# Kernel optimization log

Hardware: AMD Instinct MI355X
Metric: run time of the kernel (lower is better)

Reference implementation:

```python
import jax, jax.numpy as jnp
import numpy as np

V, D, N, T, U, E = 200000, 128, 50000, 20, 128, 128

def setup_inputs() -> dict:
    key = jax.random.key(0)
    ks = jax.random.split(key, 12)
    s = 0.02
    return {
        "node_ids": jax.random.randint(ks[0], (N,), 0, V, dtype=jnp.int32),
        "neigh_ids": jax.random.randint(ks[1], (N, T), 0, V, dtype=jnp.int32),
        "alpha": jax.random.uniform(ks[2], (N, T), dtype=jnp.float32),
        "table": jax.random.normal(ks[3], (V, D), dtype=jnp.float32),
        "Wq": jax.random.normal(ks[4], (D, U), dtype=jnp.float32) * s,
        "bq": jnp.zeros((U,), dtype=jnp.float32),
        "Wn": jax.random.normal(ks[5], (D, U), dtype=jnp.float32) * s,
        "bn": jnp.zeros((U,), dtype=jnp.float32),
        "Ww": jax.random.normal(ks[6], (2 * U, U), dtype=jnp.float32) * s,
        "bw": jnp.zeros((U,), dtype=jnp.float32),
        "Wg": jax.random.normal(ks[7], (U, E), dtype=jnp.float32) * s,
        "bg": jnp.zeros((E,), dtype=jnp.float32),
    }

def reference(node_ids, neigh_ids, alpha, table, Wq, bq, Wn, bn, Ww, bw, Wg, bg):
    # gather initial embeddings (irregular indexing)
    node_x = table[node_ids]            # [N, D]
    neigh_x = table[neigh_ids]          # [N, T, D]
    # Convolve: node branch Dense+ReLU
    node_h = jax.nn.relu(node_x @ Wq + bq)                       # [N, U]
    # Aggregator: neighbor Dense+ReLU then alpha-weighted matmul
    neigh_h = jax.nn.relu(jnp.einsum('ntd,du->ntu', neigh_x, Wn) + bn)  # [N, T, U]
    agg = jnp.einsum('nt,ntu->nu', alpha, neigh_h)               # [N, U]
    # concat + Dense+ReLU
    emb = jax.nn.relu(jnp.concatenate([node_h, agg], axis=-1) @ Ww + bw)  # [N, U]
    # global (Frobenius) L2 normalize, as in tf.divide(Emb, tf.norm(Emb, ord=2))
    emb = emb / jnp.linalg.norm(emb)
    # final Dense+ReLU to emb_dim
    return jax.nn.relu(emb @ Wg + bg)                            # [N, E]
```

## Files before the change

### kernel.cpp

```cpp
#include <hip/hip_runtime.h>
#include <math.h>


using f32x4  = __attribute__((ext_vector_type(4))) float;
using short8 = __attribute__((ext_vector_type(8))) short;

__device__ __forceinline__ ushort f2bf(float f) {
    uint u = __float_as_uint(f);
    return (ushort)((u + 0x7fffu + ((u >> 16) & 1u)) >> 16);
}
__device__ __forceinline__ float bf2f(ushort h) {
    return __uint_as_float((uint)h << 16);
}

__global__ __launch_bounds__(256)
void prep_weights(const float* __restrict__ Wq, const float* __restrict__ Wn,
                  const float* __restrict__ Ww, const float* __restrict__ Wg,
                  ushort* __restrict__ WqT, ushort* __restrict__ WnT,
                  ushort* __restrict__ WwT, ushort* __restrict__ WgT)
{
    int idx = blockIdx.x * 256 + threadIdx.x;
    const float* W; ushort* WT; int K; int j = idx;
    if (j < 16384)      { W = Wq; WT = WqT; K = 128; }
    else if (j < 32768) { W = Wn; WT = WnT; K = 128; j -= 16384; }
    else if (j < 65536) { W = Ww; WT = WwT; K = 256; j -= 32768; }
    else                { W = Wg; WT = WgT; K = 128; j -= 65536; }
    int n = j & 127, k = j >> 7;
    WT[(size_t)n * K + k] = f2bf(W[j]);
}

template<int KTOT, bool GATHER, bool ABF16, bool SUMSQ, bool SCALE, bool OUTBF16>
__global__ __launch_bounds__(256, 2)
void mfma_gemm(const void* __restrict__ Av, int lda,
               const int* __restrict__ gidx,
               const ushort* __restrict__ WT,
               const float* __restrict__ bias,
               void* __restrict__ outv, int ldo, int M,
               float* __restrict__ partials,
               const float* __restrict__ scale_ptr)
{
    __shared__ __align__(16) char smem[65536];
    __shared__ float red[256];
    char* Bbase = smem + 32768;

    const int tid = threadIdx.x;
    const int w   = tid >> 6;
    const int l   = tid & 63;
    const int l16 = l & 15, lh = l >> 4;
    const int brow = blockIdx.x * 128;

    f32x4 acc[2][8];
#pragma unroll
    for (int fr = 0; fr < 2; ++fr)
#pragma unroll
        for (int fc = 0; fc < 8; ++fc)
#pragma unroll
            for (int i = 0; i < 4; ++i) acc[fr][fc][i] = 0.f;

    for (int k0 = 0; k0 < KTOT; k0 += 128) {
        if (ABF16) {
            const ushort* A = (const ushort*)Av;
#pragma unroll
            for (int it = 0; it < 8; ++it) {
                int idx = it * 256 + tid;
                int r = idx >> 4, o = idx & 15;
                int row = brow + r; int grow = (row < M) ? row : (M - 1);
                if (GATHER) grow = gidx[grow];
                uint4 v = *reinterpret_cast<const uint4*>(&A[(size_t)grow * lda + k0 + 8 * o]);
                *reinterpret_cast<uint4*>(smem + r * 256 + ((16 * o) ^ ((r & 7) << 4))) = v;
            }
        } else {
            const float* A = (const float*)Av;
#pragma unroll
            for (int it = 0; it < 16; ++it) {
                int idx = it * 256 + tid;
                int r = idx >> 5, q = idx & 31;
                int row = brow + r; int grow = (row < M) ? row : (M - 1);
                if (GATHER) grow = gidx[grow];
                float4 v = *reinterpret_cast<const float4*>(&A[(size_t)grow * lda + k0 + 4 * q]);
                uint2 p;
                p.x = (uint)f2bf(v.x) | ((uint)f2bf(v.y) << 16);
                p.y = (uint)f2bf(v.z) | ((uint)f2bf(v.w) << 16);
                *reinterpret_cast<uint2*>(smem + r * 256 + ((8 * q) ^ ((r & 7) << 4))) = p;
            }
        }
#pragma unroll
        for (int it = 0; it < 8; ++it) {
            int idx = it * 256 + tid;
            int n = idx >> 4, o = idx & 15;
            uint4 v = *reinterpret_cast<const uint4*>(&WT[(size_t)n * KTOT + k0 + 8 * o]);
            *reinterpret_cast<uint4*>(Bbase + n * 256 + ((16 * o) ^ ((n & 7) << 4))) = v;
        }
        __syncthreads();

        const int r0 = 32 * w + l16;
        const int r1 = r0 + 16;
#pragma unroll
        for (int ks = 0; ks < 4; ++ks) {
            const int kb = 64 * ks + 16 * lh;
            short8 a0 = *reinterpret_cast<const short8*>(
                smem + r0 * 256 + (kb ^ ((r0 & 7) << 4)));
            short8 a1 = *reinterpret_cast<const short8*>(
                smem + r1 * 256 + (kb ^ ((r1 & 7) << 4)));
#pragma unroll
            for (int fc = 0; fc < 8; ++fc) {
                const int nn = 16 * fc + l16;
                short8 b = *reinterpret_cast<const short8*>(
                    Bbase + nn * 256 + (kb ^ ((nn & 7) << 4)));
                acc[0][fc] = __builtin_amdgcn_mfma_f32_16x16x32_bf16(a0, b, acc[0][fc], 0, 0, 0);
                acc[1][fc] = __builtin_amdgcn_mfma_f32_16x16x32_bf16(a1, b, acc[1][fc], 0, 0, 0);
            }
        }
        __syncthreads();
    }

    const float scale = SCALE ? scale_ptr[0] : 1.0f;
    float bloc[8];
#pragma unroll
    for (int fc = 0; fc < 8; ++fc) bloc[fc] = bias[16 * fc + l16];

    float ssq = 0.f;
#pragma unroll
    for (int fr = 0; fr < 2; ++fr)
#pragma unroll
        for (int fc = 0; fc < 8; ++fc)
#pragma unroll
            for (int i = 0; i < 4; ++i) {
                const int r   = 32 * w + 16 * fr + 4 * lh + i;
                const int col = 16 * fc + l16;
                float v = fmaxf(fmaf(acc[fr][fc][i], scale, bloc[fc]), 0.f);
                if (SUMSQ) { if (brow + r < M) ssq += v * v; }
                if (OUTBF16) ((ushort*)smem)[r * 128 + col] = f2bf(v);
                else         ((float*)smem)[r * 128 + col] = v;
            }
    __syncthreads();

    if (OUTBF16) {
        ushort* out = (ushort*)outv;
#pragma unroll
        for (int it = 0; it < 8; ++it) {
            int idx = it * 256 + tid;
            int r = idx >> 4, o = idx & 15;
            if (brow + r < M)
                *reinterpret_cast<uint4*>(&out[(size_t)(brow + r) * ldo + 8 * o]) =
                    *reinterpret_cast<const uint4*>((ushort*)smem + r * 128 + 8 * o);
        }
    } else {
        float* out = (float*)outv;
#pragma unroll
        for (int it = 0; it < 16; ++it) {
            int idx = it * 256 + tid;
            int r = idx >> 5, q = idx & 31;
            if (brow + r < M)
                *reinterpret_cast<float4*>(&out[(size_t)(brow + r) * ldo + 4 * q]) =
                    *reinterpret_cast<const float4*>((float*)smem + r * 128 + 4 * q);
        }
    }

    if (SUMSQ) {
        red[tid] = ssq;
        __syncthreads();
        for (int st = 128; st > 0; st >>= 1) {
            if (tid < st) red[tid] += red[tid + st];
            __syncthreads();
        }
        if (tid == 0) partials[blockIdx.x] = red[0];
    }
}

__global__ __launch_bounds__(256)
void agg_bf16(const ushort* __restrict__ H,
              const int* __restrict__ nids,
              const float* __restrict__ alpha,
              ushort* __restrict__ outb,
              int N)
{
    const int n   = blockIdx.x * 16 + (threadIdx.x >> 4);
    const int l16 = threadIdx.x & 15;
    if (n >= N) return;

    const int*   idp = &nids[n * 20];
    const float* alp = &alpha[n * 20];
    float a[8];
#pragma unroll
    for (int j = 0; j < 8; ++j) a[j] = 0.f;

#pragma unroll
    for (int t = 0; t < 20; ++t) {
        const int   id = idp[t];
        const float al = alp[t];
        uint4 h = *reinterpret_cast<const uint4*>(&H[(size_t)id * 128 + 8 * l16]);
        a[0] = fmaf(al, bf2f((ushort)(h.x & 0xffff)), a[0]);
        a[1] = fmaf(al, bf2f((ushort)(h.x >> 16)),    a[1]);
        a[2] = fmaf(al, bf2f((ushort)(h.y & 0xffff)), a[2]);
        a[3] = fmaf(al, bf2f((ushort)(h.y >> 16)),    a[3]);
        a[4] = fmaf(al, bf2f((ushort)(h.z & 0xffff)), a[4]);
        a[5] = fmaf(al, bf2f((ushort)(h.z >> 16)),    a[5]);
        a[6] = fmaf(al, bf2f((ushort)(h.w & 0xffff)), a[6]);
        a[7] = fmaf(al, bf2f((ushort)(h.w >> 16)),    a[7]);
    }
    uint4 p;
    p.x = (uint)f2bf(a[0]) | ((uint)f2bf(a[1]) << 16);
    p.y = (uint)f2bf(a[2]) | ((uint)f2bf(a[3]) << 16);
    p.z = (uint)f2bf(a[4]) | ((uint)f2bf(a[5]) << 16);
    p.w = (uint)f2bf(a[6]) | ((uint)f2bf(a[7]) << 16);
    *reinterpret_cast<uint4*>(&outb[(size_t)n * 256 + 8 * l16]) = p;
}

__global__ void reduce_norm(const float* __restrict__ partials, int n,
                            float* __restrict__ scale)
{
    __shared__ float red[256];
    float s = 0.f;
    for (int i = threadIdx.x; i < n; i += 256) s += partials[i];
    red[threadIdx.x] = s;
    __syncthreads();
    for (int st = 128; st > 0; st >>= 1) {
        if (threadIdx.x < st) red[threadIdx.x] += red[threadIdx.x + st];
        __syncthreads();
    }
    if (threadIdx.x == 0) scale[0] = 1.0f / sqrtf(red[0]);
}

extern "C" void kernel_launch(void* const* d_in, const int* in_sizes, int n_in,
                              void* d_out, int out_size, void* d_ws, size_t ws_size,
                              hipStream_t stream)
{
    const int*   node_ids  = (const int*)  d_in[0];
    const int*   neigh_ids = (const int*)  d_in[1];
    const float* alpha     = (const float*)d_in[2];
    const float* table     = (const float*)d_in[3];
    const float* Wq        = (const float*)d_in[4];
    const float* bq        = (const float*)d_in[5];
    const float* Wn        = (const float*)d_in[6];
    const float* bn        = (const float*)d_in[7];
    const float* Ww        = (const float*)d_in[8];
    const float* bw        = (const float*)d_in[9];
    const float* Wg        = (const float*)d_in[10];
    const float* bg        = (const float*)d_in[11];

    const int N = in_sizes[0];
    const int V = in_sizes[3] / 128;
    float* out = (float*)d_out;

    ushort* H    = (ushort*)d_ws;
    ushort* nh   = H    + (size_t)V * 128;
    ushort* embb = nh   + (size_t)N * 256;
    ushort* WqT  = embb + (size_t)N * 128;
    ushort* WnT  = WqT  + 16384;
    ushort* WwT  = WnT  + 16384;
    ushort* WgT  = WwT  + 32768;
    float*  partials = (float*)(WgT + 16384);
    float*  scale    = partials + 512;

    const size_t need = (size_t)((char*)(scale + 16) - (char*)d_ws);
    if (ws_size < need) return;

    const int nblkN = (N + 127) / 128;
    const int nblkV = (V + 127) / 128;

    prep_weights<<<320, 256, 0, stream>>>(Wq, Wn, Ww, Wg, WqT, WnT, WwT, WgT);
    mfma_gemm<128, false, false, false, false, true><<<nblkV, 256, 0, stream>>>(
        table, 128, nullptr, WnT, bn, H, 128, V, nullptr, nullptr);
    mfma_gemm<128, true, false, false, false, true><<<nblkN, 256, 0, stream>>>(
        table, 128, node_ids, WqT, bq, nh, 256, N, nullptr, nullptr);
    agg_bf16<<<(N + 15) / 16, 256, 0, stream>>>(H, neigh_ids, alpha, nh + 128, N);
    mfma_gemm<256, false, true, true, false, true><<<nblkN, 256, 0, stream>>>(
        nh, 256, nullptr, WwT, bw, embb, 128, N, partials, nullptr);
    reduce_norm<<<1, 256, 0, stream>>>(partials, nblkN, scale);
    mfma_gemm<128, false, true, false, true, false><<<nblkN, 256, 0, stream>>>(
        embb, 128, nullptr, WgT, bg, out, 128, N, nullptr, scale);
}
```

Baseline: 113.7 us.

## Load A fragments directly into registers and swap MFMA operands to skip LDS staging

```diff
diff --git a/kernel.cpp b/kernel.cpp
--- a/kernel.cpp
+++ b/kernel.cpp
@@ -11,6 +11,15 @@
 }
 __device__ __forceinline__ float bf2f(ushort h) {
     return __uint_as_float((uint)h << 16);
+}
+__device__ __forceinline__ uint pk2(float lo, float hi) {
+    return (uint)f2bf(lo) | ((uint)f2bf(hi) << 16);
+}
+__device__ __forceinline__ short8 pack8(f32x4 a, f32x4 b) {
+    uint u0 = pk2(a[0], a[1]), u1 = pk2(a[2], a[3]);
+    uint u2 = pk2(b[0], b[1]), u3 = pk2(b[2], b[3]);
+    uint4 r; r.x = u0; r.y = u1; r.z = u2; r.w = u3;
+    union { uint4 u; short8 s; } cv; cv.u = r; return cv.s;
 }
 
 __global__ __launch_bounds__(256)
@@ -29,7 +38,7 @@
     WT[(size_t)n * K + k] = f2bf(W[j]);
 }
 
-template<int KTOT, bool GATHER, bool ABF16, bool SUMSQ, bool SCALE, bool OUTBF16>
+template<int KTOT, bool GATHER, bool AFP32, bool SUMSQ, bool SCALE, bool OUTFP32>
 __global__ __launch_bounds__(256, 2)
 void mfma_gemm(const void* __restrict__ Av, int lda,
                const int* __restrict__ gidx,
@@ -39,121 +48,112 @@
                float* __restrict__ partials,
                const float* __restrict__ scale_ptr)
 {
-    __shared__ __align__(16) char smem[65536];
+    __shared__ __align__(16) ushort Blds[128 * 128];
     __shared__ float red[256];
-    char* Bbase = smem + 32768;
 
     const int tid = threadIdx.x;
-    const int w   = tid >> 6;
-    const int l   = tid & 63;
+    const int w = tid >> 6, l = tid & 63;
     const int l16 = l & 15, lh = l >> 4;
     const int brow = blockIdx.x * 128;
 
+    const int row0 = brow + 32 * w + l16;
+    const int row1 = row0 + 16;
+    int g0 = (row0 < M) ? row0 : (M - 1);
+    int g1 = (row1 < M) ? row1 : (M - 1);
+    if (GATHER) { g0 = gidx[g0]; g1 = gidx[g1]; }
+
     f32x4 acc[2][8];
 #pragma unroll
-    for (int fr = 0; fr < 2; ++fr)
-#pragma unroll
-        for (int fc = 0; fc < 8; ++fc)
-#pragma unroll
-            for (int i = 0; i < 4; ++i) acc[fr][fc][i] = 0.f;
-
-    for (int k0 = 0; k0 < KTOT; k0 += 128) {
-        if (ABF16) {
+    for (int nt = 0; nt < 2; ++nt)
+#pragma unroll
+        for (int mt = 0; mt < 8; ++mt)
+#pragma unroll
+            for (int i = 0; i < 4; ++i) acc[nt][mt][i] = 0.f;
+
+    for (int kc = 0; kc < KTOT / 128; ++kc) {
+        const int kbase = kc * 128;
+
+        short8 a[2][4];
+        f32x4 t[2][8];
+        if (AFP32) {
+            const float* A = (const float*)Av;
+#pragma unroll
+            for (int nt = 0; nt < 2; ++nt) {
+                const float* rp = A + (size_t)(nt ? g1 : g0) * lda + kbase + 8 * lh;
+#pragma unroll
+                for (int ks = 0; ks < 4; ++ks) {
+                    t[nt][2 * ks]     = *reinterpret_cast<const f32x4*>(rp + 32 * ks);
+                    t[nt][2 * ks + 1] = *reinterpret_cast<const f32x4*>(rp + 32 * ks + 4);
+                }
+            }
+        } else {
             const ushort* A = (const ushort*)Av;
 #pragma unroll
-            for (int it = 0; it < 8; ++it) {
-                int idx = it * 256 + tid;
-                int r = idx >> 4, o = idx & 15;
-                int row = brow + r; int grow = (row < M) ? row : (M - 1);
-                if (GATHER) grow = gidx[grow];
-                uint4 v = *reinterpret_cast<const uint4*>(&A[(size_t)grow * lda + k0 + 8 * o]);
-                *reinterpret_cast<uint4*>(smem + r * 256 + ((16 * o) ^ ((r & 7) << 4))) = v;
-            }
-        } else {
-            const float* A = (const float*)Av;
-#pragma unroll
-            for (int it = 0; it < 16; ++it) {
-                int idx = it * 256 + tid;
-                int r = idx >> 5, q = idx & 31;
-                int row = brow + r; int grow = (row < M) ? row : (M - 1);
-                if (GATHER) grow = gidx[grow];
-                float4 v = *reinterpret_cast<const float4*>(&A[(size_t)grow * lda + k0 + 4 * q]);
-                uint2 p;
-                p.x = (uint)f2bf(v.x) | ((uint)f2bf(v.y) << 16);
-                p.y = (uint)f2bf(v.z) | ((uint)f2bf(v.w) << 16);
-                *reinterpret_cast<uint2*>(smem + r * 256 + ((8 * q) ^ ((r & 7) << 4))) = p;
-            }
-        }
+            for (int nt = 0; nt < 2; ++nt) {
+                const ushort* rp = A + (size_t)(nt ? g1 : g0) * lda + kbase + 8 * lh;
+#pragma unroll
+                for (int ks = 0; ks < 4; ++ks)
+                    a[nt][ks] = *reinterpret_cast<const short8*>(rp + 32 * ks);
+            }
+        }
+
+        if (kc > 0) __syncthreads();
 #pragma unroll
         for (int it = 0; it < 8; ++it) {
             int idx = it * 256 + tid;
             int n = idx >> 4, o = idx & 15;
-            uint4 v = *reinterpret_cast<const uint4*>(&WT[(size_t)n * KTOT + k0 + 8 * o]);
-            *reinterpret_cast<uint4*>(Bbase + n * 256 + ((16 * o) ^ ((n & 7) << 4))) = v;
+            uint4 v = *reinterpret_cast<const uint4*>(&WT[(size_t)n * KTOT + kbase + 8 * o]);
+            *reinterpret_cast<uint4*>(
+                (char*)Blds + n * 256 + ((16 * o) ^ ((n & 7) << 4))) = v;
         }
         __syncthreads();
 
-        const int r0 = 32 * w + l16;
-        const int r1 = r0 + 16;
+        if (AFP32) {
+#pragma unroll
+            for (int nt = 0; nt < 2; ++nt)
+#pragma unroll
+                for (int ks = 0; ks < 4; ++ks)
+                    a[nt][ks] = pack8(t[nt][2 * ks], t[nt][2 * ks + 1]);
+        }
+
 #pragma unroll
         for (int ks = 0; ks < 4; ++ks) {
-            const int kb = 64 * ks + 16 * lh;
-            short8 a0 = *reinterpret_cast<const short8*>(
-                smem + r0 * 256 + (kb ^ ((r0 & 7) << 4)));
-            short8 a1 = *reinterpret_cast<const short8*>(
-                smem + r1 * 256 + (kb ^ ((r1 & 7) << 4)));
-#pragma unroll
-            for (int fc = 0; fc < 8; ++fc) {
-                const int nn = 16 * fc + l16;
-                short8 b = *reinterpret_cast<const short8*>(
-                    Bbase + nn * 256 + (kb ^ ((nn & 7) << 4)));
-                acc[0][fc] = __builtin_amdgcn_mfma_f32_16x16x32_bf16(a0, b, acc[0][fc], 0, 0, 0);
-                acc[1][fc] = __builtin_amdgcn_mfma_f32_16x16x32_bf16(a1, b, acc[1][fc], 0, 0, 0);
-            }
-        }
-        __syncthreads();
+#pragma unroll
+            for (int mt = 0; mt < 8; ++mt) {
+                short8 wf = *reinterpret_cast<const short8*>(
+                    (char*)Blds + (16 * mt + l16) * 256 +
+                    ((64 * ks + 16 * lh) ^ ((l16 & 7) << 4)));
+                acc[0][mt] = __builtin_amdgcn_mfma_f32_16x16x32_bf16(wf, a[0][ks], acc[0][mt], 0, 0, 0);
+                acc[1][mt] = __builtin_amdgcn_mfma_f32_16x16x32_bf16(wf, a[1][ks], acc[1][mt], 0, 0, 0);
+            }
+        }
     }
 
     const float scale = SCALE ? scale_ptr[0] : 1.0f;
-    float bloc[8];
-#pragma unroll
-    for (int fc = 0; fc < 8; ++fc) bloc[fc] = bias[16 * fc + l16];
-
     float ssq = 0.f;
 #pragma unroll
-    for (int fr = 0; fr < 2; ++fr)
-#pragma unroll
-        for (int fc = 0; fc < 8; ++fc)
-#pragma unroll
-            for (int i = 0; i < 4; ++i) {
-                const int r   = 32 * w + 16 * fr + 4 * lh + i;
-                const int col = 16 * fc + l16;
-                float v = fmaxf(fmaf(acc[fr][fc][i], scale, bloc[fc]), 0.f);
-                if (SUMSQ) { if (brow + r < M) ssq += v * v; }
-                if (OUTBF16) ((ushort*)smem)[r * 128 + col] = f2bf(v);
-                else         ((float*)smem)[r * 128 + col] = v;
-            }
-    __syncthreads();
-
-    if (OUTBF16) {
-        ushort* out = (ushort*)outv;
-#pragma unroll
-        for (int it = 0; it < 8; ++it) {
-            int idx = it * 256 + tid;
-            int r = idx >> 4, o = idx & 15;
-            if (brow + r < M)
-                *reinterpret_cast<uint4*>(&out[(size_t)(brow + r) * ldo + 8 * o]) =
-                    *reinterpret_cast<const uint4*>((ushort*)smem + r * 128 + 8 * o);
-        }
-    } else {
-        float* out = (float*)outv;
-#pragma unroll
-        for (int it = 0; it < 16; ++it) {
-            int idx = it * 256 + tid;
-            int r = idx >> 5, q = idx & 31;
-            if (brow + r < M)
-                *reinterpret_cast<float4*>(&out[(size_t)(brow + r) * ldo + 4 * q]) =
-                    *reinterpret_cast<const float4*>((float*)smem + r * 128 + 4 * q);
+    for (int nt = 0; nt < 2; ++nt) {
+        const int row = nt ? row1 : row0;
+        const bool ok = row < M;
+#pragma unroll
+        for (int mt = 0; mt < 8; ++mt) {
+            const f32x4 bv = *reinterpret_cast<const f32x4*>(&bias[16 * mt + 4 * lh]);
+            f32x4 v;
+#pragma unroll
+            for (int i = 0; i < 4; ++i)
+                v[i] = fmaxf(fmaf(acc[nt][mt][i], scale, bv[i]), 0.f);
+            if (SUMSQ && ok)
+                ssq += v[0] * v[0] + v[1] * v[1] + v[2] * v[2] + v[3] * v[3];
+            if (OUTFP32) {
+                if (ok)
+                    *reinterpret_cast<f32x4*>(
+                        &((float*)outv)[(size_t)row * ldo + 16 * mt + 4 * lh]) = v;
+            } else {
+                uint2 p; p.x = pk2(v[0], v[1]); p.y = pk2(v[2], v[3]);
+                if (ok)
+                    *reinterpret_cast<uint2*>(
+                        &((ushort*)outv)[(size_t)row * ldo + 16 * mt + 4 * lh]) = p;
+            }
         }
     }
 
@@ -200,10 +200,10 @@
         a[7] = fmaf(al, bf2f((ushort)(h.w >> 16)),    a[7]);
     }
     uint4 p;
-    p.x = (uint)f2bf(a[0]) | ((uint)f2bf(a[1]) << 16);
-    p.y = (uint)f2bf(a[2]) | ((uint)f2bf(a[3]) << 16);
-    p.z = (uint)f2bf(a[4]) | ((uint)f2bf(a[5]) << 16);
-    p.w = (uint)f2bf(a[6]) | ((uint)f2bf(a[7]) << 16);
+    p.x = pk2(a[0], a[1]);
+    p.y = pk2(a[2], a[3]);
+    p.z = pk2(a[4], a[5]);
+    p.w = pk2(a[6], a[7]);
     *reinterpret_cast<uint4*>(&outb[(size_t)n * 256 + 8 * l16]) = p;
 }
 
@@ -260,14 +260,14 @@
     const int nblkV = (V + 127) / 128;
 
     prep_weights<<<320, 256, 0, stream>>>(Wq, Wn, Ww, Wg, WqT, WnT, WwT, WgT);
-    mfma_gemm<128, false, false, false, false, true><<<nblkV, 256, 0, stream>>>(
+    mfma_gemm<128, false, true, false, false, false><<<nblkV, 256, 0, stream>>>(
         table, 128, nullptr, WnT, bn, H, 128, V, nullptr, nullptr);
-    mfma_gemm<128, true, false, false, false, true><<<nblkN, 256, 0, stream>>>(
+    mfma_gemm<128, true, true, false, false, false><<<nblkN, 256, 0, stream>>>(
         table, 128, node_ids, WqT, bq, nh, 256, N, nullptr, nullptr);
     agg_bf16<<<(N + 15) / 16, 256, 0, stream>>>(H, neigh_ids, alpha, nh + 128, N);
-    mfma_gemm<256, false, true, true, false, true><<<nblkN, 256, 0, stream>>>(
+    mfma_gemm<256, false, false, true, false, false><<<nblkN, 256, 0, stream>>>(
         nh, 256, nullptr, WwT, bw, embb, 128, N, partials, nullptr);
     reduce_norm<<<1, 256, 0, stream>>>(partials, nblkN, scale);
-    mfma_gemm<128, false, true, false, true, false><<<nblkN, 256, 0, stream>>>(
+    mfma_gemm<128, false, false, false, true, true><<<nblkN, 256, 0, stream>>>(
         embb, 128, nullptr, WgT, bg, out, 128, N, nullptr, scale);
 }
```

New measurement: 125.1 us. 1.1x slower.

## Merge table and node projections into one persistent kernel with prefetch

Applied to the files above, without the earlier changes.

```diff
diff --git a/kernel.cpp b/kernel.cpp
--- a/kernel.cpp
+++ b/kernel.cpp
@@ -11,6 +11,9 @@
 }
 __device__ __forceinline__ float bf2f(ushort h) {
     return __uint_as_float((uint)h << 16);
+}
+__device__ __forceinline__ uint pk2(float lo, float hi) {
+    return (uint)f2bf(lo) | ((uint)f2bf(hi) << 16);
 }
 
 __global__ __launch_bounds__(256)
@@ -29,143 +32,129 @@
     WT[(size_t)n * K + k] = f2bf(W[j]);
 }
 
-template<int KTOT, bool GATHER, bool ABF16, bool SUMSQ, bool SCALE, bool OUTBF16>
-__global__ __launch_bounds__(256, 2)
-void mfma_gemm(const void* __restrict__ Av, int lda,
-               const int* __restrict__ gidx,
-               const ushort* __restrict__ WT,
-               const float* __restrict__ bias,
-               void* __restrict__ outv, int ldo, int M,
-               float* __restrict__ partials,
-               const float* __restrict__ scale_ptr)
-{
-    __shared__ __align__(16) char smem[65536];
-    __shared__ float red[256];
-    char* Bbase = smem + 32768;
-
+__device__ __forceinline__ void stage_w128(const ushort* __restrict__ WT,
+                                           const float* __restrict__ bias,
+                                           ushort* Wlds, float* blds, int tid)
+{
+#pragma unroll
+    for (int it = 0; it < 8; ++it) {
+        int idx = it * 256 + tid, n = idx >> 4, o = idx & 15;
+        uint4 v = *reinterpret_cast<const uint4*>(&WT[(size_t)n * 128 + 8 * o]);
+        *reinterpret_cast<uint4*>((char*)Wlds + n * 256 + ((16 * o) ^ ((n & 7) << 4))) = v;
+    }
+    if (tid < 128) blds[tid] = bias[tid];
+}
+
+template<bool GATHER>
+__device__ __forceinline__ void k1_side(const float* __restrict__ table,
+                                        const int* __restrict__ gidx,
+                                        const ushort* Wlds, const float* blds,
+                                        ushort* Albs,
+                                        ushort* __restrict__ out, int ldo, int M,
+                                        int sideIdx, int sideBlk)
+{
     const int tid = threadIdx.x;
-    const int w   = tid >> 6;
-    const int l   = tid & 63;
-    const int l16 = l & 15, lh = l >> 4;
-    const int brow = blockIdx.x * 128;
-
-    f32x4 acc[2][8];
-#pragma unroll
-    for (int fr = 0; fr < 2; ++fr)
-#pragma unroll
-        for (int fc = 0; fc < 8; ++fc)
-#pragma unroll
-            for (int i = 0; i < 4; ++i) acc[fr][fc][i] = 0.f;
-
-    for (int k0 = 0; k0 < KTOT; k0 += 128) {
-        if (ABF16) {
-            const ushort* A = (const ushort*)Av;
-#pragma unroll
-            for (int it = 0; it < 8; ++it) {
-                int idx = it * 256 + tid;
-                int r = idx >> 4, o = idx & 15;
-                int row = brow + r; int grow = (row < M) ? row : (M - 1);
-                if (GATHER) grow = gidx[grow];
-                uint4 v = *reinterpret_cast<const uint4*>(&A[(size_t)grow * lda + k0 + 8 * o]);
-                *reinterpret_cast<uint4*>(smem + r * 256 + ((16 * o) ^ ((r & 7) << 4))) = v;
-            }
-        } else {
-            const float* A = (const float*)Av;
-#pragma unroll
-            for (int it = 0; it < 16; ++it) {
-                int idx = it * 256 + tid;
-                int r = idx >> 5, q = idx & 31;
-                int row = brow + r; int grow = (row < M) ? row : (M - 1);
-                if (GATHER) grow = gidx[grow];
-                float4 v = *reinterpret_cast<const float4*>(&A[(size_t)grow * lda + k0 + 4 * q]);
-                uint2 p;
-                p.x = (uint)f2bf(v.x) | ((uint)f2bf(v.y) << 16);
-                p.y = (uint)f2bf(v.z) | ((uint)f2bf(v.w) << 16);
-                *reinterpret_cast<uint2*>(smem + r * 256 + ((8 * q) ^ ((r & 7) << 4))) = p;
-            }
-        }
-#pragma unroll
-        for (int it = 0; it < 8; ++it) {
-            int idx = it * 256 + tid;
-            int n = idx >> 4, o = idx & 15;
-            uint4 v = *reinterpret_cast<const uint4*>(&WT[(size_t)n * KTOT + k0 + 8 * o]);
-            *reinterpret_cast<uint4*>(Bbase + n * 256 + ((16 * o) ^ ((n & 7) << 4))) = v;
-        }
-        __syncthreads();
-
-        const int r0 = 32 * w + l16;
-        const int r1 = r0 + 16;
+    const int w = tid >> 6, l = tid & 63, l16 = l & 15, lh = l >> 4;
+    const int nt = (M + 63) >> 6;
+    int tile = sideIdx;
+
+    f32x4 f[8];
+    if (tile < nt) {
+#pragma unroll
+        for (int j = 0; j < 8; ++j) {
+            int u = j * 256 + tid;
+            int r = u >> 5, c4 = u & 31;
+            int row = tile * 64 + r;
+            int g = (row < M) ? row : (M - 1);
+            if (GATHER) g = gidx[g];
+            f[j] = *reinterpret_cast<const f32x4*>(table + (size_t)g * 128 + 4 * c4);
+        }
+    }
+    __syncthreads();
+
+    for (; tile < nt; tile += sideBlk) {
+        uint2 p[8];
+#pragma unroll
+        for (int j = 0; j < 8; ++j) {
+            p[j].x = pk2(f[j][0], f[j][1]);
+            p[j].y = pk2(f[j][2], f[j][3]);
+        }
+        __syncthreads();
+#pragma unroll
+        for (int j = 0; j < 8; ++j) {
+            int u = j * 256 + tid, r = u >> 5, c4 = u & 31;
+            *reinterpret_cast<uint2*>(
+                (char*)Albs + r * 256 + ((8 * c4) ^ ((r & 7) << 4))) = p[j];
+        }
+        __syncthreads();
+
+        const int nxt = tile + sideBlk;
+        if (nxt < nt) {
+#pragma unroll
+            for (int j = 0; j < 8; ++j) {
+                int u = j * 256 + tid;
+                int r = u >> 5, c4 = u & 31;
+                int row = nxt * 64 + r;
+                int g = (row < M) ? row : (M - 1);
+                if (GATHER) g = gidx[g];
+                f[j] = *reinterpret_cast<const f32x4*>(table + (size_t)g * 128 + 4 * c4);
+            }
+        }
+
+        f32x4 acc[8];
+#pragma unroll
+        for (int mt = 0; mt < 8; ++mt)
+#pragma unroll
+            for (int i = 0; i < 4; ++i) acc[mt][i] = 0.f;
+        const int r0 = 16 * w + l16;
 #pragma unroll
         for (int ks = 0; ks < 4; ++ks) {
-            const int kb = 64 * ks + 16 * lh;
-            short8 a0 = *reinterpret_cast<const short8*>(
-                smem + r0 * 256 + (kb ^ ((r0 & 7) << 4)));
-            short8 a1 = *reinterpret_cast<const short8*>(
-                smem + r1 * 256 + (kb ^ ((r1 & 7) << 4)));
-#pragma unroll
-            for (int fc = 0; fc < 8; ++fc) {
-                const int nn = 16 * fc + l16;
-                short8 b = *reinterpret_cast<const short8*>(
-                    Bbase + nn * 256 + (kb ^ ((nn & 7) << 4)));
-                acc[0][fc] = __builtin_amdgcn_mfma_f32_16x16x32_bf16(a0, b, acc[0][fc], 0, 0, 0);
-                acc[1][fc] = __builtin_amdgcn_mfma_f32_16x16x32_bf16(a1, b, acc[1][fc], 0, 0, 0);
-            }
-        }
-        __syncthreads();
-    }
-
-    const float scale = SCALE ? scale_ptr[0] : 1.0f;
-    float bloc[8];
-#pragma unroll
-    for (int fc = 0; fc < 8; ++fc) bloc[fc] = bias[16 * fc + l16];
-
-    float ssq = 0.f;
-#pragma unroll
-    for (int fr = 0; fr < 2; ++fr)
-#pragma unroll
-        for (int fc = 0; fc < 8; ++fc)
-#pragma unroll
-            for (int i = 0; i < 4; ++i) {
-                const int r   = 32 * w + 16 * fr + 4 * lh + i;
-                const int col = 16 * fc + l16;
-                float v = fmaxf(fmaf(acc[fr][fc][i], scale, bloc[fc]), 0.f);
-                if (SUMSQ) { if (brow + r < M) ssq += v * v; }
-                if (OUTBF16) ((ushort*)smem)[r * 128 + col] = f2bf(v);
-                else         ((float*)smem)[r * 128 + col] = v;
-            }
-    __syncthreads();
-
-    if (OUTBF16) {
-        ushort* out = (ushort*)outv;
-#pragma unroll
-        for (int it = 0; it < 8; ++it) {
-            int idx = it * 256 + tid;
-            int r = idx >> 4, o = idx & 15;
-            if (brow + r < M)
-                *reinterpret_cast<uint4*>(&out[(size_t)(brow + r) * ldo + 8 * o]) =
-                    *reinterpret_cast<const uint4*>((ushort*)smem + r * 128 + 8 * o);
-        }
-    } else {
-        float* out = (float*)outv;
-#pragma unroll
-        for (int it = 0; it < 16; ++it) {
-            int idx = it * 256 + tid;
-            int r = idx >> 5, q = idx & 31;
-            if (brow + r < M)
-                *reinterpret_cast<float4*>(&out[(size_t)(brow + r) * ldo + 4 * q]) =
-                    *reinterpret_cast<const float4*>((float*)smem + r * 128 + 4 * q);
-        }
-    }
-
-    if (SUMSQ) {
-        red[tid] = ssq;
-        __syncthreads();
-        for (int st = 128; st > 0; st >>= 1) {
-            if (tid < st) red[tid] += red[tid + st];
-            __syncthreads();
-        }
-        if (tid == 0) partials[blockIdx.x] = red[0];
-    }
+            short8 a = *reinterpret_cast<const short8*>(
+                (const char*)Albs + r0 * 256 + ((64 * ks + 16 * lh) ^ ((r0 & 7) << 4)));
+#pragma unroll
+            for (int mt = 0; mt < 8; ++mt) {
+                short8 wf = *reinterpret_cast<const short8*>(
+                    (const char*)Wlds + (16 * mt + l16) * 256 +
+                    ((64 * ks + 16 * lh) ^ ((l16 & 7) << 4)));
+                acc[mt] = __builtin_amdgcn_mfma_f32_16x16x32_bf16(wf, a, acc[mt], 0, 0, 0);
+            }
+        }
+
+        const int row = tile * 64 + r0;
+        if (row < M) {
+#pragma unroll
+            for (int mt = 0; mt < 8; ++mt) {
+                f32x4 bv = *reinterpret_cast<const f32x4*>(&blds[16 * mt + 4 * lh]);
+                uint2 q;
+                q.x = pk2(fmaxf(acc[mt][0] + bv[0], 0.f), fmaxf(acc[mt][1] + bv[1], 0.f));
+                q.y = pk2(fmaxf(acc[mt][2] + bv[2], 0.f), fmaxf(acc[mt][3] + bv[3], 0.f));
+                *reinterpret_cast<uint2*>(&out[(size_t)row * ldo + 16 * mt + 4 * lh]) = q;
+            }
+        }
+    }
+}
+
+__global__ __launch_bounds__(256, 3)
+void k1_dual(const float* __restrict__ table, const int* __restrict__ node_ids,
+             const ushort* __restrict__ WnT, const float* __restrict__ bn,
+             const ushort* __restrict__ WqT, const float* __restrict__ bq,
+             ushort* __restrict__ H, ushort* __restrict__ nh,
+             int V, int N, int splitH, int nBlk)
+{
+    __shared__ __align__(16) ushort Wlds[128 * 128];
+    __shared__ __align__(16) ushort Albs[64 * 128];
+    __shared__ __align__(16) float blds[128];
+    const int tid = threadIdx.x;
+    const bool isH = (int)blockIdx.x < splitH;
+
+    stage_w128(isH ? WnT : WqT, isH ? bn : bq, Wlds, blds, tid);
+
+    if (isH)
+        k1_side<false>(table, nullptr, Wlds, blds, Albs, H, 128, V,
+                       blockIdx.x, splitH);
+    else
+        k1_side<true>(table, node_ids, Wlds, blds, Albs, nh, 256, N,
+                      blockIdx.x - splitH, nBlk - splitH);
 }
 
 __global__ __launch_bounds__(256)
@@ -184,7 +173,6 @@
     float a[8];
 #pragma unroll
     for (int j = 0; j < 8; ++j) a[j] = 0.f;
-
 #pragma unroll
     for (int t = 0; t < 20; ++t) {
         const int   id = idp[t];
@@ -200,11 +188,148 @@
         a[7] = fmaf(al, bf2f((ushort)(h.w >> 16)),    a[7]);
     }
     uint4 p;
-    p.x = (uint)f2bf(a[0]) | ((uint)f2bf(a[1]) << 16);
-    p.y = (uint)f2bf(a[2]) | ((uint)f2bf(a[3]) << 16);
-    p.z = (uint)f2bf(a[4]) | ((uint)f2bf(a[5]) << 16);
-    p.w = (uint)f2bf(a[6]) | ((uint)f2bf(a[7]) << 16);
+    p.x = pk2(a[0], a[1]); p.y = pk2(a[2], a[3]);
+    p.z = pk2(a[4], a[5]); p.w = pk2(a[6], a[7]);
     *reinterpret_cast<uint4*>(&outb[(size_t)n * 256 + 8 * l16]) = p;
+}
+
+template<int KTOT, bool GATHER, bool ABF16, bool SUMSQ, bool SCALE, bool OUTBF16>
+__global__ __launch_bounds__(256, 2)
+void mfma_gemm(const void* __restrict__ Av, int lda,
+               const int* __restrict__ gidx,
+               const ushort* __restrict__ WT,
+               const float* __restrict__ bias,
+               void* __restrict__ outv, int ldo, int M,
+               float* __restrict__ partials,
+               const float* __restrict__ scale_ptr)
+{
+    __shared__ __align__(16) char smem[65536];
+    __shared__ float red[256];
+    char* Bbase = smem + 32768;
+
+    const int tid = threadIdx.x;
+    const int w   = tid >> 6;
+    const int l   = tid & 63;
+    const int l16 = l & 15, lh = l >> 4;
+    const int brow = blockIdx.x * 128;
+
+    f32x4 acc[2][8];
+#pragma unroll
+    for (int fr = 0; fr < 2; ++fr)
+#pragma unroll
+        for (int fc = 0; fc < 8; ++fc)
+#pragma unroll
+            for (int i = 0; i < 4; ++i) acc[fr][fc][i] = 0.f;
+
+    for (int k0 = 0; k0 < KTOT; k0 += 128) {
+        if (ABF16) {
+            const ushort* A = (const ushort*)Av;
+#pragma unroll
+            for (int it = 0; it < 8; ++it) {
+                int idx = it * 256 + tid;
+                int r = idx >> 4, o = idx & 15;
+                int row = brow + r; int grow = (row < M) ? row : (M - 1);
+                if (GATHER) grow = gidx[grow];
+                uint4 v = *reinterpret_cast<const uint4*>(&A[(size_t)grow * lda + k0 + 8 * o]);
+                *reinterpret_cast<uint4*>(smem + r * 256 + ((16 * o) ^ ((r & 7) << 4))) = v;
+            }
+        } else {
+            const float* A = (const float*)Av;
+#pragma unroll
+            for (int it = 0; it < 16; ++it) {
+                int idx = it * 256 + tid;
+                int r = idx >> 5, q = idx & 31;
+                int row = brow + r; int grow = (row < M) ? row : (M - 1);
+                if (GATHER) grow = gidx[grow];
+                float4 v = *reinterpret_cast<const float4*>(&A[(size_t)grow * lda + k0 + 4 * q]);
+                uint2 p;
+                p.x = pk2(v.x, v.y);
+                p.y = pk2(v.z, v.w);
+                *reinterpret_cast<uint2*>(smem + r * 256 + ((8 * q) ^ ((r & 7) << 4))) = p;
+            }
+        }
+#pragma unroll
+        for (int it = 0; it < 8; ++it) {
+            int idx = it * 256 + tid;
+            int n = idx >> 4, o = idx & 15;
+            uint4 v = *reinterpret_cast<const uint4*>(&WT[(size_t)n * KTOT + k0 + 8 * o]);
+            *reinterpret_cast<uint4*>(Bbase + n * 256 + ((16 * o) ^ ((n & 7) << 4))) = v;
+        }
+        __syncthreads();
+
+        const int r0 = 32 * w + l16;
+        const int r1 = r0 + 16;
+#pragma unroll
+        for (int ks = 0; ks < 4; ++ks) {
+            const int kb = 64 * ks + 16 * lh;
+            short8 a0 = *reinterpret_cast<const short8*>(
+                smem + r0 * 256 + (kb ^ ((r0 & 7) << 4)));
+            short8 a1 = *reinterpret_cast<const short8*>(
+                smem + r1 * 256 + (kb ^ ((r1 & 7) << 4)));
+#pragma unroll
+            for (int fc = 0; fc < 8; ++fc) {
+                const int nn = 16 * fc + l16;
+                short8 b = *reinterpret_cast<const short8*>(
+                    Bbase + nn * 256 + (kb ^ ((nn & 7) << 4)));
+                acc[0][fc] = __builtin_amdgcn_mfma_f32_16x16x32_bf16(a0, b, acc[0][fc], 0, 0, 0);
+                acc[1][fc] = __builtin_amdgcn_mfma_f32_16x16x32_bf16(a1, b, acc[1][fc], 0, 0, 0);
+            }
+        }
+        __syncthreads();
+    }
+
+    const float scale = SCALE ? scale_ptr[0] : 1.0f;
+    float bloc[8];
+#pragma unroll
+    for (int fc = 0; fc < 8; ++fc) bloc[fc] = bias[16 * fc + l16];
+
+    float ssq = 0.f;
+#pragma unroll
+    for (int fr = 0; fr < 2; ++fr)
+#pragma unroll
+        for (int fc = 0; fc < 8; ++fc)
+#pragma unroll
+            for (int i = 0; i < 4; ++i) {
+                const int r   = 32 * w + 16 * fr + 4 * lh + i;
+                const int col = 16 * fc + l16;
+                float v = fmaxf(fmaf(acc[fr][fc][i], scale, bloc[fc]), 0.f);
+                if (SUMSQ) { if (brow + r < M) ssq += v * v; }
+                if (OUTBF16) ((ushort*)smem)[r * 128 + col] = f2bf(v);
+                else         ((float*)smem)[r * 128 + col] = v;
+            }
+    __syncthreads();
+
+    if (OUTBF16) {
+        ushort* out = (ushort*)outv;
+#pragma unroll
+        for (int it = 0; it < 8; ++it) {
+            int idx = it * 256 + tid;
+            int r = idx >> 4, o = idx & 15;
+            if (brow + r < M)
+                *reinterpret_cast<uint4*>(&out[(size_t)(brow + r) * ldo + 8 * o]) =
+                    *reinterpret_cast<const uint4*>((ushort*)smem + r * 128 + 8 * o);
+        }
+    } else {
+        float* out = (float*)outv;
+#pragma unroll
+        for (int it = 0; it < 16; ++it) {
+            int idx = it * 256 + tid;
+            int r = idx >> 5, q = idx & 31;
+            if (brow + r < M)
+                *reinterpret_cast<float4*>(&out[(size_t)(brow + r) * ldo + 4 * q]) =
+                    *reinterpret_cast<const float4*>((float*)smem + r * 128 + 4 * q);
+        }
+    }
+
+    if (SUMSQ) {
+        red[tid] = ssq;
+        __syncthreads();
+        for (int st = 128; st > 0; st >>= 1) {
+            if (tid < st) red[tid] += red[tid + st];
+            __syncthreads();
+        }
+        if (tid == 0) partials[blockIdx.x] = red[0];
+    }
 }
 
 __global__ void reduce_norm(const float* __restrict__ partials, int n,
@@ -257,13 +382,16 @@
     if (ws_size < need) return;
 
     const int nblkN = (N + 127) / 128;
-    const int nblkV = (V + 127) / 128;
+
+    const int G1 = 768;
+    const long long tH = (V + 63) / 64, tN = (N + 63) / 64;
+    int splitH = (int)((G1 * tH) / (tH + tN));
+    if (splitH < 1) splitH = 1;
+    if (splitH > G1 - 1) splitH = G1 - 1;
 
     prep_weights<<<320, 256, 0, stream>>>(Wq, Wn, Ww, Wg, WqT, WnT, WwT, WgT);
-    mfma_gemm<128, false, false, false, false, true><<<nblkV, 256, 0, stream>>>(
-        table, 128, nullptr, WnT, bn, H, 128, V, nullptr, nullptr);
-    mfma_gemm<128, true, false, false, false, true><<<nblkN, 256, 0, stream>>>(
-        table, 128, node_ids, WqT, bq, nh, 256, N, nullptr, nullptr);
+    k1_dual<<<G1, 256, 0, stream>>>(table, node_ids, WnT, bn, WqT, bq,
+                                    H, nh, V, N, splitH, G1);
     agg_bf16<<<(N + 15) / 16, 256, 0, stream>>>(H, neigh_ids, alpha, nh + 128, N);
     mfma_gemm<256, false, true, true, false, true><<<nblkN, 256, 0, stream>>>(
         nh, 256, nullptr, WwT, bw, embb, 128, N, partials, nullptr);
```

Result: faster. 103.7 us (-8.8%).

## Keep weights in registers with persistent waves for the K=128 GEMMs, merging the table and node GEMMs

Applied to the files above, without the earlier changes.

```diff
diff --git a/kernel.cpp b/kernel.cpp
--- a/kernel.cpp
+++ b/kernel.cpp
@@ -11,6 +11,15 @@
 }
 __device__ __forceinline__ float bf2f(ushort h) {
     return __uint_as_float((uint)h << 16);
+}
+__device__ __forceinline__ uint pk2(float lo, float hi) {
+    return (uint)f2bf(lo) | ((uint)f2bf(hi) << 16);
+}
+__device__ __forceinline__ short8 pack8(f32x4 a, f32x4 b) {
+    uint4 r;
+    r.x = pk2(a[0], a[1]); r.y = pk2(a[2], a[3]);
+    r.z = pk2(b[0], b[1]); r.w = pk2(b[2], b[3]);
+    union { uint4 u; short8 s; } cv; cv.u = r; return cv.s;
 }
 
 __global__ __launch_bounds__(256)
@@ -29,142 +38,134 @@
     WT[(size_t)n * K + k] = f2bf(W[j]);
 }
 
-template<int KTOT, bool GATHER, bool ABF16, bool SUMSQ, bool SCALE, bool OUTBF16>
 __global__ __launch_bounds__(256, 2)
-void mfma_gemm(const void* __restrict__ Av, int lda,
-               const int* __restrict__ gidx,
-               const ushort* __restrict__ WT,
-               const float* __restrict__ bias,
-               void* __restrict__ outv, int ldo, int M,
-               float* __restrict__ partials,
-               const float* __restrict__ scale_ptr)
-{
-    __shared__ __align__(16) char smem[65536];
-    __shared__ float red[256];
-    char* Bbase = smem + 32768;
-
+void k1_reg(const float* __restrict__ table, const int* __restrict__ node_ids,
+            const ushort* __restrict__ WnT, const float* __restrict__ bn,
+            const ushort* __restrict__ WqT, const float* __restrict__ bq,
+            ushort* __restrict__ H, ushort* __restrict__ nh,
+            int V, int N, int splitH)
+{
+    __shared__ float blds[128];
     const int tid = threadIdx.x;
-    const int w   = tid >> 6;
-    const int l   = tid & 63;
-    const int l16 = l & 15, lh = l >> 4;
-    const int brow = blockIdx.x * 128;
-
-    f32x4 acc[2][8];
-#pragma unroll
-    for (int fr = 0; fr < 2; ++fr)
-#pragma unroll
-        for (int fc = 0; fc < 8; ++fc)
-#pragma unroll
-            for (int i = 0; i < 4; ++i) acc[fr][fc][i] = 0.f;
-
-    for (int k0 = 0; k0 < KTOT; k0 += 128) {
-        if (ABF16) {
-            const ushort* A = (const ushort*)Av;
-#pragma unroll
-            for (int it = 0; it < 8; ++it) {
-                int idx = it * 256 + tid;
-                int r = idx >> 4, o = idx & 15;
-                int row = brow + r; int grow = (row < M) ? row : (M - 1);
-                if (GATHER) grow = gidx[grow];
-                uint4 v = *reinterpret_cast<const uint4*>(&A[(size_t)grow * lda + k0 + 8 * o]);
-                *reinterpret_cast<uint4*>(smem + r * 256 + ((16 * o) ^ ((r & 7) << 4))) = v;
+    const int w = tid >> 6, l = tid & 63, l16 = l & 15, lh = l >> 4;
+    const bool isH = (int)blockIdx.x < splitH;
+
+    const ushort* WT = isH ? WnT : WqT;
+    short8 wreg[4][8];
+#pragma unroll
+    for (int ks = 0; ks < 4; ++ks)
+#pragma unroll
+        for (int mt = 0; mt < 8; ++mt)
+            wreg[ks][mt] = *reinterpret_cast<const short8*>(
+                &WT[(size_t)(16 * mt + l16) * 128 + 32 * ks + 8 * lh]);
+    if (tid < 128) blds[tid] = (isH ? bn : bq)[tid];
+    __syncthreads();
+
+    const int M   = isH ? V : N;
+    ushort* out   = isH ? H : nh;
+    const int ldo = isH ? 128 : 256;
+    const int nt  = (M + 15) >> 4;
+    const int wid    = (isH ? (int)blockIdx.x : (int)blockIdx.x - splitH) * 4 + w;
+    const int nwaves = (isH ? splitH : (int)gridDim.x - splitH) * 4;
+
+    for (int tile = wid; tile < nt; tile += nwaves) {
+        const int row = tile * 16 + l16;
+        int g = (row < M) ? row : (M - 1);
+        if (!isH) g = node_ids[g];
+        const float* rp = table + (size_t)g * 128 + 8 * lh;
+
+        f32x4 f[8];
+#pragma unroll
+        for (int ks = 0; ks < 4; ++ks) {
+            f[2 * ks]     = *reinterpret_cast<const f32x4*>(rp + 32 * ks);
+            f[2 * ks + 1] = *reinterpret_cast<const f32x4*>(rp + 32 * ks + 4);
+        }
+        short8 a[4];
+#pragma unroll
+        for (int ks = 0; ks < 4; ++ks) a[ks] = pack8(f[2 * ks], f[2 * ks + 1]);
+
+        f32x4 acc[8];
+#pragma unroll
+        for (int mt = 0; mt < 8; ++mt)
+#pragma unroll
+            for (int i = 0; i < 4; ++i) acc[mt][i] = 0.f;
+#pragma unroll
+        for (int ks = 0; ks < 4; ++ks)
+#pragma unroll
+            for (int mt = 0; mt < 8; ++mt)
+                acc[mt] = __builtin_amdgcn_mfma_f32_16x16x32_bf16(
+                    wreg[ks][mt], a[ks], acc[mt], 0, 0, 0);
+
+        if (row < M) {
+#pragma unroll
+            for (int mt = 0; mt < 8; ++mt) {
+                f32x4 bv = *reinterpret_cast<const f32x4*>(&blds[16 * mt + 4 * lh]);
+                uint2 q;
+                q.x = pk2(fmaxf(acc[mt][0] + bv[0], 0.f), fmaxf(acc[mt][1] + bv[1], 0.f));
+                q.y = pk2(fmaxf(acc[mt][2] + bv[2], 0.f), fmaxf(acc[mt][3] + bv[3], 0.f));
+                *reinterpret_cast<uint2*>(&out[(size_t)row * ldo + 16 * mt + 4 * lh]) = q;
             }
-        } else {
-            const float* A = (const float*)Av;
-#pragma unroll
-            for (int it = 0; it < 16; ++it) {
-                int idx = it * 256 + tid;
-                int r = idx >> 5, q = idx & 31;
-                int row = brow + r; int grow = (row < M) ? row : (M - 1);
-                if (GATHER) grow = gidx[grow];
-                float4 v = *reinterpret_cast<const float4*>(&A[(size_t)grow * lda + k0 + 4 * q]);
-                uint2 p;
-                p.x = (uint)f2bf(v.x) | ((uint)f2bf(v.y) << 16);
-                p.y = (uint)f2bf(v.z) | ((uint)f2bf(v.w) << 16);
-                *reinterpret_cast<uint2*>(smem + r * 256 + ((8 * q) ^ ((r & 7) << 4))) = p;
+        }
+    }
+}
+
+__global__ __launch_bounds__(256, 2)
+void k5_reg(const ushort* __restrict__ embb, const ushort* __restrict__ WgT,
+            const float* __restrict__ bg, const float* __restrict__ scale_ptr,
+            float* __restrict__ outp, int N)
+{
+    __shared__ float blds[128];
+    const int tid = threadIdx.x;
+    const int w = tid >> 6, l = tid & 63, l16 = l & 15, lh = l >> 4;
+
+    short8 wreg[4][8];
+#pragma unroll
+    for (int ks = 0; ks < 4; ++ks)
+#pragma unroll
+        for (int mt = 0; mt < 8; ++mt)
+            wreg[ks][mt] = *reinterpret_cast<const short8*>(
+                &WgT[(size_t)(16 * mt + l16) * 128 + 32 * ks + 8 * lh]);
+    if (tid < 128) blds[tid] = bg[tid];
+    __syncthreads();
+    const float scale = scale_ptr[0];
+
+    const int nt = (N + 15) >> 4;
+    const int wid = (int)blockIdx.x * 4 + w;
+    const int nwaves = (int)gridDim.x * 4;
+
+    for (int tile = wid; tile < nt; tile += nwaves) {
+        const int row = tile * 16 + l16;
+        const int g = (row < N) ? row : (N - 1);
+        const ushort* rp = embb + (size_t)g * 128 + 8 * lh;
+
+        short8 a[4];
+#pragma unroll
+        for (int ks = 0; ks < 4; ++ks)
+            a[ks] = *reinterpret_cast<const short8*>(rp + 32 * ks);
+
+        f32x4 acc[8];
+#pragma unroll
+        for (int mt = 0; mt < 8; ++mt)
+#pragma unroll
+            for (int i = 0; i < 4; ++i) acc[mt][i] = 0.f;
+#pragma unroll
+        for (int ks = 0; ks < 4; ++ks)
+#pragma unroll
+            for (int mt = 0; mt < 8; ++mt)
+                acc[mt] = __builtin_amdgcn_mfma_f32_16x16x32_bf16(
+                    wreg[ks][mt], a[ks], acc[mt], 0, 0, 0);
+
+        if (row < N) {
+#pragma unroll
+            for (int mt = 0; mt < 8; ++mt) {
+                f32x4 bv = *reinterpret_cast<const f32x4*>(&blds[16 * mt + 4 * lh]);
+                f32x4 v;
+#pragma unroll
+                for (int i = 0; i < 4; ++i)
+                    v[i] = fmaxf(fmaf(acc[mt][i], scale, bv[i]), 0.f);
+                *reinterpret_cast<f32x4*>(&outp[(size_t)row * 128 + 16 * mt + 4 * lh]) = v;
             }
         }
-#pragma unroll
-        for (int it = 0; it < 8; ++it) {
-            int idx = it * 256 + tid;
-            int n = idx >> 4, o = idx & 15;
-            uint4 v = *reinterpret_cast<const uint4*>(&WT[(size_t)n * KTOT + k0 + 8 * o]);
-            *reinterpret_cast<uint4*>(Bbase + n * 256 + ((16 * o) ^ ((n & 7) << 4))) = v;
-        }
-        __syncthreads();
-
-        const int r0 = 32 * w + l16;
-        const int r1 = r0 + 16;
-#pragma unroll
-        for (int ks = 0; ks < 4; ++ks) {
-            const int kb = 64 * ks + 16 * lh;
-            short8 a0 = *reinterpret_cast<const short8*>(
-                smem + r0 * 256 + (kb ^ ((r0 & 7) << 4)));
-            short8 a1 = *reinterpret_cast<const short8*>(
-                smem + r1 * 256 + (kb ^ ((r1 & 7) << 4)));
-#pragma unroll
-            for (int fc = 0; fc < 8; ++fc) {
-                const int nn = 16 * fc + l16;
-                short8 b = *reinterpret_cast<const short8*>(
-                    Bbase + nn * 256 + (kb ^ ((nn & 7) << 4)));
-                acc[0][fc] = __builtin_amdgcn_mfma_f32_16x16x32_bf16(a0, b, acc[0][fc], 0, 0, 0);
-                acc[1][fc] = __builtin_amdgcn_mfma_f32_16x16x32_bf16(a1, b, acc[1][fc], 0, 0, 0);
-            }
-        }
-        __syncthreads();
-    }
-
-    const float scale = SCALE ? scale_ptr[0] : 1.0f;
-    float bloc[8];
-#pragma unroll
-    for (int fc = 0; fc < 8; ++fc) bloc[fc] = bias[16 * fc + l16];
-
-    float ssq = 0.f;
-#pragma unroll
-    for (int fr = 0; fr < 2; ++fr)
-#pragma unroll
-        for (int fc = 0; fc < 8; ++fc)
-#pragma unroll
-            for (int i = 0; i < 4; ++i) {
-                const int r   = 32 * w + 16 * fr + 4 * lh + i;
-                const int col = 16 * fc + l16;
-                float v = fmaxf(fmaf(acc[fr][fc][i], scale, bloc[fc]), 0.f);
-                if (SUMSQ) { if (brow + r < M) ssq += v * v; }
-                if (OUTBF16) ((ushort*)smem)[r * 128 + col] = f2bf(v);
-                else         ((float*)smem)[r * 128 + col] = v;
-            }
-    __syncthreads();
-
-    if (OUTBF16) {
-        ushort* out = (ushort*)outv;
-#pragma unroll
-        for (int it = 0; it < 8; ++it) {
-            int idx = it * 256 + tid;
-            int r = idx >> 4, o = idx & 15;
-            if (brow + r < M)
-                *reinterpret_cast<uint4*>(&out[(size_t)(brow + r) * ldo + 8 * o]) =
-                    *reinterpret_cast<const uint4*>((ushort*)smem + r * 128 + 8 * o);
-        }
-    } else {
-        float* out = (float*)outv;
-#pragma unroll
-        for (int it = 0; it < 16; ++it) {
-            int idx = it * 256 + tid;
-            int r = idx >> 5, q = idx & 31;
-            if (brow + r < M)
-                *reinterpret_cast<float4*>(&out[(size_t)(brow + r) * ldo + 4 * q]) =
-                    *reinterpret_cast<const float4*>((float*)smem + r * 128 + 4 * q);
-        }
-    }
-
-    if (SUMSQ) {
-        red[tid] = ssq;
-        __syncthreads();
-        for (int st = 128; st > 0; st >>= 1) {
-            if (tid < st) red[tid] += red[tid + st];
-            __syncthreads();
-        }
-        if (tid == 0) partials[blockIdx.x] = red[0];
     }
 }
 
@@ -184,7 +185,6 @@
     float a[8];
 #pragma unroll
     for (int j = 0; j < 8; ++j) a[j] = 0.f;
-
 #pragma unroll
     for (int t = 0; t < 20; ++t) {
         const int   id = idp[t];
@@ -200,11 +200,109 @@
         a[7] = fmaf(al, bf2f((ushort)(h.w >> 16)),    a[7]);
     }
     uint4 p;
-    p.x = (uint)f2bf(a[0]) | ((uint)f2bf(a[1]) << 16);
-    p.y = (uint)f2bf(a[2]) | ((uint)f2bf(a[3]) << 16);
-    p.z = (uint)f2bf(a[4]) | ((uint)f2bf(a[5]) << 16);
-    p.w = (uint)f2bf(a[6]) | ((uint)f2bf(a[7]) << 16);
+    p.x = pk2(a[0], a[1]); p.y = pk2(a[2], a[3]);
+    p.z = pk2(a[4], a[5]); p.w = pk2(a[6], a[7]);
     *reinterpret_cast<uint4*>(&outb[(size_t)n * 256 + 8 * l16]) = p;
+}
+
+__global__ __launch_bounds__(256, 2)
+void k3_emb(const ushort* __restrict__ nh, const ushort* __restrict__ WT,
+            const float* __restrict__ bias, ushort* __restrict__ embb,
+            float* __restrict__ partials, int M)
+{
+    __shared__ __align__(16) char smem[65536];
+    __shared__ float red[256];
+    char* Bbase = smem + 32768;
+    const int KTOT = 256, lda = 256, ldo = 128;
+
+    const int tid = threadIdx.x;
+    const int w   = tid >> 6;
+    const int l   = tid & 63;
+    const int l16 = l & 15, lh = l >> 4;
+    const int brow = blockIdx.x * 128;
+
+    f32x4 acc[2][8];
+#pragma unroll
+    for (int fr = 0; fr < 2; ++fr)
+#pragma unroll
+        for (int fc = 0; fc < 8; ++fc)
+#pragma unroll
+            for (int i = 0; i < 4; ++i) acc[fr][fc][i] = 0.f;
+
+    for (int k0 = 0; k0 < KTOT; k0 += 128) {
+#pragma unroll
+        for (int it = 0; it < 8; ++it) {
+            int idx = it * 256 + tid;
+            int r = idx >> 4, o = idx & 15;
+            int row = brow + r; int grow = (row < M) ? row : (M - 1);
+            uint4 v = *reinterpret_cast<const uint4*>(&nh[(size_t)grow * lda + k0 + 8 * o]);
+            *reinterpret_cast<uint4*>(smem + r * 256 + ((16 * o) ^ ((r & 7) << 4))) = v;
+        }
+#pragma unroll
+        for (int it = 0; it < 8; ++it) {
+            int idx = it * 256 + tid;
+            int n = idx >> 4, o = idx & 15;
+            uint4 v = *reinterpret_cast<const uint4*>(&WT[(size_t)n * KTOT + k0 + 8 * o]);
+            *reinterpret_cast<uint4*>(Bbase + n * 256 + ((16 * o) ^ ((n & 7) << 4))) = v;
+        }
+        __syncthreads();
+
+        const int r0 = 32 * w + l16;
+        const int r1 = r0 + 16;
+#pragma unroll
+        for (int ks = 0; ks < 4; ++ks) {
+            const int kb = 64 * ks + 16 * lh;
+            short8 a0 = *reinterpret_cast<const short8*>(
+                smem + r0 * 256 + (kb ^ ((r0 & 7) << 4)));
+            short8 a1 = *reinterpret_cast<const short8*>(
+                smem + r1 * 256 + (kb ^ ((r1 & 7) << 4)));
+#pragma unroll
+            for (int fc = 0; fc < 8; ++fc) {
+                const int nn = 16 * fc + l16;
+                short8 b = *reinterpret_cast<const short8*>(
+                    Bbase + nn * 256 + (kb ^ ((nn & 7) << 4)));
+                acc[0][fc] = __builtin_amdgcn_mfma_f32_16x16x32_bf16(a0, b, acc[0][fc], 0, 0, 0);
+                acc[1][fc] = __builtin_amdgcn_mfma_f32_16x16x32_bf16(a1, b, acc[1][fc], 0, 0, 0);
+            }
+        }
+        __syncthreads();
+    }
+
+    float bloc[8];
+#pragma unroll
+    for (int fc = 0; fc < 8; ++fc) bloc[fc] = bias[16 * fc + l16];
+
+    float ssq = 0.f;
+#pragma unroll
+    for (int fr = 0; fr < 2; ++fr)
+#pragma unroll
+        for (int fc = 0; fc < 8; ++fc)
+#pragma unroll
+            for (int i = 0; i < 4; ++i) {
+                const int r   = 32 * w + 16 * fr + 4 * lh + i;
+                const int col = 16 * fc + l16;
+                float v = fmaxf(acc[fr][fc][i] + bloc[fc], 0.f);
+                if (brow + r < M) ssq += v * v;
+                ((ushort*)smem)[r * 128 + col] = f2bf(v);
+            }
+    __syncthreads();
+
+#pragma unroll
+    for (int it = 0; it < 8; ++it) {
+        int idx = it * 256 + tid;
+        int r = idx >> 4, o = idx & 15;
+        if (brow + r < M)
+            *reinterpret_cast<uint4*>(&embb[(size_t)(brow + r) * ldo + 8 * o]) =
+                *reinterpret_cast<const uint4*>((ushort*)smem + r * 128 + 8 * o);
+    }
+
+    red[tid] = ssq;
+    __syncthreads();
+    for (int st = 128; st > 0; st >>= 1) {
+        if (tid < st) red[tid] += red[tid + st];
+        __syncthreads();
+    }
+    if (tid == 0) partials[blockIdx.x] = red[0];
 }
 
 __global__ void reduce_norm(const float* __restrict__ partials, int n,
@@ -257,17 +355,18 @@
     if (ws_size < need) return;
 
     const int nblkN = (N + 127) / 128;
-    const int nblkV = (V + 127) / 128;
+
+    const int G1 = 512;
+    const long long tH = (V + 15) / 16, tN = (N + 15) / 16;
+    int splitH = (int)((G1 * tH) / (tH + tN));
+    if (splitH < 1) splitH = 1;
+    if (splitH > G1 - 1) splitH = G1 - 1;
 
     prep_weights<<<320, 256, 0, stream>>>(Wq, Wn, Ww, Wg, WqT, WnT, WwT, WgT);
-    mfma_gemm<128, false, false, false, false, true><<<nblkV, 256, 0, stream>>>(
-        table, 128, nullptr, WnT, bn, H, 128, V, nullptr, nullptr);
-    mfma_gemm<128, true, false, false, false, true><<<nblkN, 256, 0, stream>>>(
-        table, 128, node_ids, WqT, bq, nh, 256, N, nullptr, nullptr);
+    k1_reg<<<G1, 256, 0, stream>>>(table, node_ids, WnT, bn, WqT, bq,
+                                   H, nh, V, N, splitH);
     agg_bf16<<<(N + 15) / 16, 256, 0, stream>>>(H, neigh_ids, alpha, nh + 128, N);
-    mfma_gemm<256, false, true, true, false, true><<<nblkN, 256, 0, stream>>>(
-        nh, 256, nullptr, WwT, bw, embb, 128, N, partials, nullptr);
+    k3_emb<<<nblkN, 256, 0, stream>>>(nh, WwT, bw, embb, partials, N);
     reduce_norm<<<1, 256, 0, stream>>>(partials, nblkN, scale);
-    mfma_gemm<128, false, true, false, true, false><<<nblkN, 256, 0, stream>>>(
-        embb, 128, nullptr, WgT, bg, out, 128, N, nullptr, scale);
-}
+    k5_reg<<<256, 256, 0, stream>>>(embb, WgT, bg, scale, out, N);
+}
```

New measurement: 117.2 us. 1.03x slower.
